# Kernel optimization log

Measured on AMD Instinct MI355X. Metric: run time of the kernel, lower is better.

Reference implementation:

```python
import jax, jax.numpy as jnp
import numpy as np

B, S, E = 2, 2048, 2048
H, D = 16, 128           # n_heads, head_dim (= rope_dim)
BASE = 10000.0


def _rope_tables(seq_len, dim):
    inv_freq = 1.0 / (BASE ** (jnp.arange(0, dim, 2, dtype=jnp.float32) / dim))
    t = jnp.arange(seq_len, dtype=jnp.float32)
    freqs = jnp.outer(t, inv_freq)                 # [S, D/2]
    emb = jnp.concatenate([freqs, freqs], axis=-1)  # [S, D]
    cos = jnp.cos(emb)[None, :, None, :]            # [1, S, 1, D]
    sin = jnp.sin(emb)[None, :, None, :]
    return cos, sin


def _rotate_half(x):
    x1, x2 = x[..., : x.shape[-1] // 2], x[..., x.shape[-1] // 2:]
    return jnp.concatenate([-x2, x1], axis=-1)


def setup_inputs() -> dict:
    key = jax.random.key(0)
    ks = jax.random.split(key, 9)
    s = 1.0 / np.sqrt(E)
    return {
        "x": jax.random.normal(ks[0], (B, S, E), dtype=jnp.float32),
        "Wq": jax.random.uniform(ks[1], (E, E), jnp.float32, -s, s),
        "bq": jax.random.uniform(ks[2], (E,), jnp.float32, -s, s),
        "Wk": jax.random.uniform(ks[3], (E, E), jnp.float32, -s, s),
        "bk": jax.random.uniform(ks[4], (E,), jnp.float32, -s, s),
        "Wv": jax.random.uniform(ks[5], (E, E), jnp.float32, -s, s),
        "bv": jax.random.uniform(ks[6], (E,), jnp.float32, -s, s),
        "Wp": jax.random.uniform(ks[7], (E, E), jnp.float32, -s, s),
        "bp": jax.random.uniform(ks[8], (E,), jnp.float32, -s, s),
    }


def reference(x, Wq, bq, Wk, bk, Wv, bv, Wp, bp):
    b, s, e = x.shape
    # QKV projections (torch Linear: y = x W^T + b)
    q = (jnp.einsum("bse,fe->bsf", x, Wq) + bq).reshape(b, s, H, D)
    k = (jnp.einsum("bse,fe->bsf", x, Wk) + bk).reshape(b, s, H, D)
    v = (jnp.einsum("bse,fe->bsf", x, Wv) + bv).reshape(b, s, H, D)
    # RoPE (rope_dim == head_dim, start_pos = 0)
    cos, sin = _rope_tables(s, D)
    q = q * cos + _rotate_half(q) * sin
    k = k * cos + _rotate_half(k) * sin
    # attention scores [b, m, n, h]
    att = jnp.einsum("bmhd,bnhd->bmnh", q, k)
    causal = jnp.tril(jnp.ones((s, s), dtype=bool))[None, :, :, None]
    att = jnp.where(causal, att, -jnp.inf)
    att = jax.nn.softmax(att / np.sqrt(D), axis=2)
    out = jnp.einsum("bmnh,bnhd->bmhd", att, v).reshape(b, s, e)
    return jnp.einsum("bse,fe->bsf", out, Wp) + bp
```

## Files before the change

kernel.cpp:

```cpp
#include <hip/hip_runtime.h>
#include <hip/hip_bf16.h>
#include <math.h>

#define BB 2
#define SS 2048
#define EE 2048
#define HH 16
#define DD 128
#define MM (BB*SS)

typedef __attribute__((ext_vector_type(8))) short bf16x8;
typedef __attribute__((ext_vector_type(4))) float f32x4;
typedef __attribute__((ext_vector_type(16))) float f32x16;
typedef __attribute__((ext_vector_type(4))) unsigned u32x4;

__device__ inline float bf2f(const __hip_bfloat16 h){ return __bfloat162float(h); }
__device__ inline __hip_bfloat16 f2bf(float f){ return __float2bfloat16(f); }
__device__ inline short f2bs(float f){
  union { __hip_bfloat16 h; short s; } u; u.h = __float2bfloat16(f); return u.s;
}
__device__ inline unsigned pk2(float a, float b){
  union { __hip_bfloat162 h2; unsigned u; } x;
  x.h2 = __float22bfloat162_rn(float2{a,b}); return x.u;
}

__device__ inline void gload16(const void* g, void* l){
  __builtin_amdgcn_global_load_lds((const __attribute__((address_space(1))) void*)g,
      (__attribute__((address_space(3))) void*)l, 16, 0, 0);
}

__global__ void cvt_kernel(const float* __restrict__ in, __hip_bfloat16* __restrict__ out, int n4){
  int i = blockIdx.x*256 + threadIdx.x;
  if (i >= n4) return;
  float4 v = ((const float4*)in)[i];
  union { short4 s4; short s[4]; } u;
  u.s[0] = f2bs(v.x); u.s[1] = f2bs(v.y); u.s[2] = f2bs(v.z); u.s[3] = f2bs(v.w);
  ((short4*)out)[i] = u.s4;
}

struct P4 { const float* s0; const float* s1; const float* s2; const float* s3;
            __hip_bfloat16* d0; __hip_bfloat16* d1; __hip_bfloat16* d2; __hip_bfloat16* d3; };
__global__ void cvt4_kernel(P4 p, int n4){
  int w = blockIdx.y;
  const float* in = w==0 ? p.s0 : w==1 ? p.s1 : w==2 ? p.s2 : p.s3;
  __hip_bfloat16* out = w==0 ? p.d0 : w==1 ? p.d1 : w==2 ? p.d2 : p.d3;
  int i = blockIdx.x*256 + threadIdx.x;
  if (i >= n4) return;
  float4 v = ((const float4*)in)[i];
  union { short4 s4; short s[4]; } u;
  u.s[0] = f2bs(v.x); u.s[1] = f2bs(v.y); u.s[2] = f2bs(v.z); u.s[3] = f2bs(v.w);
  ((short4*)out)[i] = u.s4;
}

__global__ void rope_tables_kernel(float* __restrict__ cost, float* __restrict__ sint){
  int idx = blockIdx.x*256 + threadIdx.x;
  int s = idx >> 6, i = idx & 63;
  double inv = exp(-log(10000.0) * (double)i / 64.0);
  double f = (double)s * inv;
  cost[idx] = (float)cos(f);
  sint[idx] = (float)sin(f);
}

__global__ void rope_kernel(__hip_bfloat16* __restrict__ q, __hip_bfloat16* __restrict__ k,
                            const float* __restrict__ cost, const float* __restrict__ sint){
  int idx = blockIdx.x*256 + threadIdx.x;
  int i = idx & 63;
  int h = (idx >> 6) & (HH-1);
  int bs = idx >> 10;
  int s = bs & (SS-1);
  float c = cost[s*64 + i], sn = sint[s*64 + i];
  size_t base = ((size_t)bs*HH + h)*DD + i;
  float q1 = bf2f(q[base]), q2 = bf2f(q[base+64]);
  q[base]    = f2bf(q1*c - q2*sn);
  q[base+64] = f2bf(q2*c + q1*sn);
  float k1 = bf2f(k[base]), k2 = bf2f(k[base+64]);
  k[base]    = f2bf(k1*c - k2*sn);
  k[base+64] = f2bf(k2*c + k1*sn);
}

template<int MODE>
__global__ __launch_bounds__(512) void gemm256(const __hip_bfloat16* __restrict__ A,
        const __hip_bfloat16* __restrict__ Bw, const float* __restrict__ bias,
        void* __restrict__ Cout){
  __shared__ __align__(1024) char lds[98304];
  const int tid = threadIdx.x, wid = tid>>6, lane = tid&63, g = lane>>4, c16 = lane&15;
  const int wm = wid>>2, wn = wid&3;
  const int orig = blockIdx.x;
  const int wg = (orig & 7)*32 + (orig >> 3);
  const int bm = wg & 31, bn = wg >> 5;
  const int rowA0 = bm*128, rowB0 = bn*256;
  const char* Ab8 = (const char*)A + (size_t)rowA0*4096;
  const char* Bb8 = (const char*)Bw + (size_t)rowB0*4096;

  f32x4 acc[4][4] = {};

  auto stage = [&](int t, int b){
    char* ad = lds + b*49152;
    char* bd = lds + b*49152 + 16384;
    #pragma unroll
    for (int i=0;i<2;i++){
      int off = i*8192 + tid*16;
      int r = off >> 7;
      int cs = (off & 127) ^ ((r&7)<<4);
      gload16(Ab8 + (size_t)r*4096 + t*128 + cs, ad + i*8192 + wid*1024);
    }
    #pragma unroll
    for (int i=0;i<4;i++){
      int off = i*8192 + tid*16;
      int r = off >> 7;
      int cs = (off & 127) ^ ((r&7)<<4);
      gload16(Bb8 + (size_t)r*4096 + t*128 + cs, bd + i*8192 + wid*1024);
    }
  };

  auto compute = [&](int b){
    const char* Abuf = lds + b*49152;
    const char* Bbuf = lds + b*49152 + 16384;
    bf16x8 bfr[4][2];
    #pragma unroll
    for (int ni=0;ni<4;ni++){
      int r = wn*64 + ni*16 + c16;
      int sw = (r&7)<<4;
      #pragma unroll
      for (int kk=0;kk<2;kk++)
        bfr[ni][kk] = *(const bf16x8*)(Bbuf + r*128 + ((kk*64 + g*16) ^ sw));
    }
    #pragma unroll
    for (int mi=0;mi<4;mi++){
      int r = wm*64 + mi*16 + c16;
      int sw = (r&7)<<4;
      bf16x8 af0 = *(const bf16x8*)(Abuf + r*128 + ((g*16) ^ sw));
      bf16x8 af1 = *(const bf16x8*)(Abuf + r*128 + ((64 + g*16) ^ sw));
      __builtin_amdgcn_s_setprio(1);
      #pragma unroll
      for (int ni=0;ni<4;ni++){
        acc[mi][ni] = __builtin_amdgcn_mfma_f32_16x16x32_bf16(af0, bfr[ni][0], acc[mi][ni],0,0,0);
        acc[mi][ni] = __builtin_amdgcn_mfma_f32_16x16x32_bf16(af1, bfr[ni][1], acc[mi][ni],0,0,0);
      }
      __builtin_amdgcn_s_setprio(0);
    }
  };

  stage(0,0);
  stage(1,1);
  asm volatile("s_waitcnt vmcnt(6)" ::: "memory");
  asm volatile("s_barrier" ::: "memory");

  #pragma unroll 1
  for (int tt = 0; tt < 32; tt += 2){
    compute(0);
    asm volatile("s_barrier" ::: "memory");
    if (tt + 2 < 32){ stage(tt+2, 0); asm volatile("s_waitcnt vmcnt(6)" ::: "memory"); }
    else            {                 asm volatile("s_waitcnt vmcnt(0)" ::: "memory"); }
    asm volatile("s_barrier" ::: "memory");
    compute(1);
    if (tt + 2 < 32){
      asm volatile("s_barrier" ::: "memory");
      if (tt + 3 < 32){ stage(tt+3, 1); asm volatile("s_waitcnt vmcnt(6)" ::: "memory"); }
      else            {                 asm volatile("s_waitcnt vmcnt(0)" ::: "memory"); }
      asm volatile("s_barrier" ::: "memory");
    }
  }

  #pragma unroll
  for (int mi=0;mi<4;mi++){
    #pragma unroll
    for (int ni=0;ni<4;ni++){
      int f = rowB0 + wn*64 + ni*16 + c16;
      float bv = bias[f];
      #pragma unroll
      for (int j=0;j<4;j++){
        int m = rowA0 + wm*64 + mi*16 + g*4 + j;
        float v = acc[mi][ni][j] + bv;
        if constexpr (MODE == 0) {
          ((__hip_bfloat16*)Cout)[(size_t)m*EE + f] = f2bf(v);
        } else if constexpr (MODE == 1) {
          int b = m >> 11, s = m & (SS-1);
          ((__hip_bfloat16*)Cout)[((size_t)(b*EE + f))*SS + s] = f2bf(v);
        } else {
          ((float*)Cout)[(size_t)m*EE + f] = v;
        }
      }
    }
  }
}

__global__ __launch_bounds__(256, 2) void attn_kernel(const __hip_bfloat16* __restrict__ qg,
    const __hip_bfloat16* __restrict__ kg, const __hip_bfloat16* __restrict__ vtg,
    __hip_bfloat16* __restrict__ og){
  __shared__ short Ks[2][64*128];
  __shared__ short Vs[2][128*64];
  const int tid=threadIdx.x, wid=tid>>6, lane=tid&63;
  const int c32 = lane & 31, hi = lane >> 5;
  const int id = blockIdx.x;
  const int u = id & 255;
  const int bh = u & 31, pr = u >> 5;
  const int qtile = (id < 256) ? (15 - pr) : pr;
  const int b = bh >> 4, h = bh & 15;
  const int q0 = qtile*128, qw = q0 + wid*32;
  const int qglob = qw + c32;
  const int niter = 2*qtile + 2;

  const char* kb8 = (const char*)(kg + ((size_t)b*SS)*EE + h*DD);
  const char* vb8 = (const char*)(vtg + (size_t)bh*DD*SS);
  const float SCL = 0.08838834764831845f * 1.4426950408889634f;

  const char* qrow = (const char*)(qg + ((size_t)(b*SS + qglob))*EE + h*DD);
  bf16x8 qf[8];
  #pragma unroll
  for (int s=0;s<8;s++) qf[s] = *(const bf16x8*)(qrow + s*32 + hi*16);

  f32x16 pacc[4] = {};
  float mrun = -INFINITY, lrun = 0.f;

  auto stageK = [&](int kv, int buf){
    #pragma unroll
    for (int i=0;i<4;i++){
      int base = i*4096 + wid*1024;
      int lb = base + lane*16;
      int r = lb >> 8, cb = lb & 255;
      gload16(kb8 + (size_t)(kv + r)*4096 + (cb ^ ((r&7)<<4)), (char*)Ks[buf] + base);
    }
  };
  auto stageV = [&](int kv, int buf){
    #pragma unroll
    for (int i=0;i<4;i++){
      int base = i*4096 + wid*1024;
      int lb = base + lane*16;
      int d = lb >> 7, cb = lb & 127;
      gload16(vb8 + (size_t)d*4096 + (size_t)kv*2 + (cb ^ ((d&7)<<4)), (char*)Vs[buf] + base);
    }
  };

  stageK(0,0); stageV(0,0);
  __syncthreads();

  int cur = 0;
  #pragma unroll 1
  for (int it = 0; it < niter; ++it){
    const int kv0 = it*64;
    if (it + 1 < niter){ stageK(kv0+64, cur^1); stageV(kv0+64, cur^1); }

    f32x16 st0 = {}, st1 = {};
    {
      const char* Kb = (const char*)Ks[cur];
      const int sw = (c32 & 7) << 4;
      #pragma unroll
      for (int s=0;s<8;s++){
        bf16x8 kf0 = *(const bf16x8*)(Kb + c32*256        + ((s*32 + hi*16) ^ sw));
        bf16x8 kf1 = *(const bf16x8*)(Kb + (32+c32)*256   + ((s*32 + hi*16) ^ sw));
        st0 = __builtin_amdgcn_mfma_f32_32x32x16_bf16(kf0, qf[s], st0, 0,0,0);
        st1 = __builtin_amdgcn_mfma_f32_32x32x16_bf16(kf1, qf[s], st1, 0,0,0);
      }
    }

    float p[32];
    float vmax = -INFINITY;
    const bool domask = (kv0 + 63 > qw);
    #pragma unroll
    for (int r=0;r<16;r++){
      float v0 = st0[r], v1 = st1[r];
      if (domask){
        int kvo = (r&3) + 8*(r>>2) + 4*hi;
        if (kv0 + kvo > qglob)      v0 = -INFINITY;
        if (kv0 + 32 + kvo > qglob) v1 = -INFINITY;
      }
      p[r] = v0; p[16+r] = v1;
      vmax = fmaxf(vmax, fmaxf(v0, v1));
    }
    vmax = fmaxf(vmax, __shfl_xor(vmax, 32));
    const float mnew = fmaxf(mrun, vmax);
    const float rs = exp2f((mrun - mnew)*SCL);
    mrun = mnew;
    float ps = 0.f;
    #pragma unroll
    for (int i=0;i<32;i++){
      p[i] = exp2f((p[i] - mnew)*SCL);
      ps += p[i];
    }
    ps += __shfl_xor(ps, 32);
    lrun = lrun*rs + ps;

    #pragma unroll
    for (int ds=0; ds<4; ds++)
      #pragma unroll
      for (int r=0;r<16;r++) pacc[ds][r] *= rs;

    unsigned w[2][4][2];
    #pragma unroll
    for (int T=0;T<2;T++)
      #pragma unroll
      for (int m=0;m<4;m++)
        #pragma unroll
        for (int uu=0;uu<2;uu++)
          w[T][m][uu] = pk2(p[T*16 + 4*m + 2*uu], p[T*16 + 4*m + 2*uu + 1]);

    bf16x8 pf[4];
    #pragma unroll
    for (int ks=0; ks<4; ks++){
      int T = ks>>1, lo2 = (ks&1)*2;
      unsigned o0 = hi ? w[T][lo2+1][0] : w[T][lo2+0][0];
      unsigned o1 = hi ? w[T][lo2+1][1] : w[T][lo2+0][1];
      unsigned s0 = hi ? w[T][lo2+0][0] : w[T][lo2+1][0];
      unsigned s1 = hi ? w[T][lo2+0][1] : w[T][lo2+1][1];
      unsigned r0 = (unsigned)__shfl_xor((int)s0, 32);
      unsigned r1 = (unsigned)__shfl_xor((int)s1, 32);
      union { u32x4 u4; bf16x8 h8; } cvt;
      cvt.u4[0] = hi ? r0 : o0;
      cvt.u4[1] = hi ? r1 : o1;
      cvt.u4[2] = hi ? o0 : r0;
      cvt.u4[3] = hi ? o1 : r1;
      pf[ks] = cvt.h8;
    }

    {
      const char* Vb = (const char*)Vs[cur];
      const int vsw = (c32 & 7) << 4;
      #pragma unroll
      for (int ds=0; ds<4; ds++){
        const char* vr = Vb + (ds*32 + c32)*128;
        #pragma unroll
        for (int ks=0; ks<4; ks++){
          bf16x8 vf = *(const bf16x8*)(vr + ((ks*32 + hi*16) ^ vsw));
          pacc[ds] = __builtin_amdgcn_mfma_f32_32x32x16_bf16(vf, pf[ks], pacc[ds], 0,0,0);
        }
      }
    }

    __syncthreads();
    cur ^= 1;
  }

  const float invl = 1.0f / lrun;
  char* orow = (char*)(og + ((size_t)(b*SS + qglob))*EE + h*DD);
  #pragma unroll
  for (int ds=0; ds<4; ds++){
    #pragma unroll
    for (int m=0;m<4;m++){
      int d0 = ds*32 + 8*m + 4*hi;
      short4 s4;
      s4.x = f2bs(pacc[ds][4*m+0]*invl);
      s4.y = f2bs(pacc[ds][4*m+1]*invl);
      s4.z = f2bs(pacc[ds][4*m+2]*invl);
      s4.w = f2bs(pacc[ds][4*m+3]*invl);
      *(short4*)(orow + d0*2) = s4;
    }
  }
}

extern "C" void kernel_launch(void* const* d_in, const int* in_sizes, int n_in,
                              void* d_out, int out_size, void* d_ws, size_t ws_size,
                              hipStream_t stream){
  const float* x  = (const float*)d_in[0];
  const float* Wq = (const float*)d_in[1];
  const float* bq = (const float*)d_in[2];
  const float* Wk = (const float*)d_in[3];
  const float* bk = (const float*)d_in[4];
  const float* Wv = (const float*)d_in[5];
  const float* bv = (const float*)d_in[6];
  const float* Wp = (const float*)d_in[7];
  const float* bp = (const float*)d_in[8];
  float* out = (float*)d_out;

  char* ws = (char*)d_ws;
  size_t off = 0;
  auto alloc = [&](size_t bytes){ void* p = ws + off; off += (bytes + 255) & ~(size_t)255; return p; };
  const size_t nx = (size_t)MM*EE;
  const size_t nw = (size_t)EE*EE;
  __hip_bfloat16* xb  = (__hip_bfloat16*)alloc(nx*2);
  __hip_bfloat16* wqb = (__hip_bfloat16*)alloc(nw*2);
  __hip_bfloat16* wkb = (__hip_bfloat16*)alloc(nw*2);
  __hip_bfloat16* wvb = (__hip_bfloat16*)alloc(nw*2);
  __hip_bfloat16* wpb = (__hip_bfloat16*)alloc(nw*2);
  __hip_bfloat16* qb  = (__hip_bfloat16*)alloc(nx*2);
  __hip_bfloat16* kb  = (__hip_bfloat16*)alloc(nx*2);
  __hip_bfloat16* vtb = (__hip_bfloat16*)alloc(nx*2);
  __hip_bfloat16* ob  = (__hip_bfloat16*)alloc(nx*2);
  float* cost = (float*)alloc((size_t)SS*64*4);
  float* sint = (float*)alloc((size_t)SS*64*4);

  cvt_kernel<<<(int)(nx/4/256), 256, 0, stream>>>(x, xb, (int)(nx/4));
  P4 p4{Wq, Wk, Wv, Wp, wqb, wkb, wvb, wpb};
  cvt4_kernel<<<dim3((int)(nw/4/256), 4), 256, 0, stream>>>(p4, (int)(nw/4));
  rope_tables_kernel<<<SS*64/256, 256, 0, stream>>>(cost, sint);

  gemm256<0><<<256, 512, 0, stream>>>(xb, wqb, bq, qb);
  gemm256<0><<<256, 512, 0, stream>>>(xb, wkb, bk, kb);
  gemm256<1><<<256, 512, 0, stream>>>(xb, wvb, bv, vtb);

  rope_kernel<<<(BB*SS*HH*64)/256, 256, 0, stream>>>(qb, kb, cost, sint);

  attn_kernel<<<dim3(512), 256, 0, stream>>>(qb, kb, vtb, ob);

  gemm256<2><<<256, 512, 0, stream>>>(ob, wpb, bp, out);
}
```

Measured before the change: 284.6 us.

## Widen attention blocks to 256 queries with paired causal tiles per block

The attention kernel now launches 256 blocks of 512 threads (8 waves). Each block covers a 256-row query tile and loops over two tiles (pp and 7-pp) so every block has balanced causal work. This doubles K/V reuse per shared-memory stage and removes the old split into 512 blocks. It also skips the online-softmax rescale when no wave lane sees a new max, and splits the exp-sum into four partial accumulators. The cost is fewer resident blocks per CU and a larger pipeline prologue per tile.

```diff
diff --git a/kernel.cpp b/kernel.cpp
--- a/kernel.cpp
+++ b/kernel.cpp
@@ -185,7 +185,7 @@
   }
 }
 
-__global__ __launch_bounds__(256, 2) void attn_kernel(const __hip_bfloat16* __restrict__ qg,
+__global__ __launch_bounds__(512, 1) void attn_kernel(const __hip_bfloat16* __restrict__ qg,
     const __hip_bfloat16* __restrict__ kg, const __hip_bfloat16* __restrict__ vtg,
     __hip_bfloat16* __restrict__ og){
   __shared__ short Ks[2][64*128];
@@ -193,30 +193,17 @@
   const int tid=threadIdx.x, wid=tid>>6, lane=tid&63;
   const int c32 = lane & 31, hi = lane >> 5;
   const int id = blockIdx.x;
-  const int u = id & 255;
-  const int bh = u & 31, pr = u >> 5;
-  const int qtile = (id < 256) ? (15 - pr) : pr;
+  const int bh = id & 31, pp = id >> 5;
   const int b = bh >> 4, h = bh & 15;
-  const int q0 = qtile*128, qw = q0 + wid*32;
-  const int qglob = qw + c32;
-  const int niter = 2*qtile + 2;
 
   const char* kb8 = (const char*)(kg + ((size_t)b*SS)*EE + h*DD);
   const char* vb8 = (const char*)(vtg + (size_t)bh*DD*SS);
   const float SCL = 0.08838834764831845f * 1.4426950408889634f;
 
-  const char* qrow = (const char*)(qg + ((size_t)(b*SS + qglob))*EE + h*DD);
-  bf16x8 qf[8];
-  #pragma unroll
-  for (int s=0;s<8;s++) qf[s] = *(const bf16x8*)(qrow + s*32 + hi*16);
-
-  f32x16 pacc[4] = {};
-  float mrun = -INFINITY, lrun = 0.f;
-
   auto stageK = [&](int kv, int buf){
     #pragma unroll
-    for (int i=0;i<4;i++){
-      int base = i*4096 + wid*1024;
+    for (int i=0;i<2;i++){
+      int base = i*8192 + wid*1024;
       int lb = base + lane*16;
       int r = lb >> 8, cb = lb & 255;
       gload16(kb8 + (size_t)(kv + r)*4096 + (cb ^ ((r&7)<<4)), (char*)Ks[buf] + base);
@@ -224,127 +211,153 @@
   };
   auto stageV = [&](int kv, int buf){
     #pragma unroll
-    for (int i=0;i<4;i++){
-      int base = i*4096 + wid*1024;
+    for (int i=0;i<2;i++){
+      int base = i*8192 + wid*1024;
       int lb = base + lane*16;
       int d = lb >> 7, cb = lb & 127;
       gload16(vb8 + (size_t)d*4096 + (size_t)kv*2 + (cb ^ ((d&7)<<4)), (char*)Vs[buf] + base);
     }
   };
 
-  stageK(0,0); stageV(0,0);
-  __syncthreads();
-
-  int cur = 0;
   #pragma unroll 1
-  for (int it = 0; it < niter; ++it){
-    const int kv0 = it*64;
-    if (it + 1 < niter){ stageK(kv0+64, cur^1); stageV(kv0+64, cur^1); }
-
-    f32x16 st0 = {}, st1 = {};
-    {
-      const char* Kb = (const char*)Ks[cur];
-      const int sw = (c32 & 7) << 4;
-      #pragma unroll
-      for (int s=0;s<8;s++){
-        bf16x8 kf0 = *(const bf16x8*)(Kb + c32*256        + ((s*32 + hi*16) ^ sw));
-        bf16x8 kf1 = *(const bf16x8*)(Kb + (32+c32)*256   + ((s*32 + hi*16) ^ sw));
-        st0 = __builtin_amdgcn_mfma_f32_32x32x16_bf16(kf0, qf[s], st0, 0,0,0);
-        st1 = __builtin_amdgcn_mfma_f32_32x32x16_bf16(kf1, qf[s], st1, 0,0,0);
-      }
-    }
-
-    float p[32];
-    float vmax = -INFINITY;
-    const bool domask = (kv0 + 63 > qw);
-    #pragma unroll
-    for (int r=0;r<16;r++){
-      float v0 = st0[r], v1 = st1[r];
-      if (domask){
-        int kvo = (r&3) + 8*(r>>2) + 4*hi;
-        if (kv0 + kvo > qglob)      v0 = -INFINITY;
-        if (kv0 + 32 + kvo > qglob) v1 = -INFINITY;
-      }
-      p[r] = v0; p[16+r] = v1;
-      vmax = fmaxf(vmax, fmaxf(v0, v1));
-    }
-    vmax = fmaxf(vmax, __shfl_xor(vmax, 32));
-    const float mnew = fmaxf(mrun, vmax);
-    const float rs = exp2f((mrun - mnew)*SCL);
-    mrun = mnew;
-    float ps = 0.f;
-    #pragma unroll
-    for (int i=0;i<32;i++){
-      p[i] = exp2f((p[i] - mnew)*SCL);
-      ps += p[i];
-    }
-    ps += __shfl_xor(ps, 32);
-    lrun = lrun*rs + ps;
-
-    #pragma unroll
-    for (int ds=0; ds<4; ds++)
-      #pragma unroll
-      for (int r=0;r<16;r++) pacc[ds][r] *= rs;
-
-    unsigned w[2][4][2];
-    #pragma unroll
-    for (int T=0;T<2;T++)
-      #pragma unroll
-      for (int m=0;m<4;m++)
+  for (int tt = 0; tt < 2; ++tt){
+    const int qtile = tt ? (7 - pp) : pp;
+    const int q0 = qtile*256, qw = q0 + wid*32;
+    const int qglob = qw + c32;
+    const int niter = 4*(qtile + 1);
+
+    const char* qrow = (const char*)(qg + ((size_t)(b*SS + qglob))*EE + h*DD);
+    bf16x8 qf[8];
+    #pragma unroll
+    for (int s=0;s<8;s++) qf[s] = *(const bf16x8*)(qrow + s*32 + hi*16);
+
+    f32x16 pacc[4] = {};
+    float mrun = -INFINITY, lrun = 0.f;
+
+    stageK(0,0); stageV(0,0);
+    __syncthreads();
+
+    int cur = 0;
+    #pragma unroll 1
+    for (int it = 0; it < niter; ++it){
+      const int kv0 = it*64;
+      if (it + 1 < niter){ stageK(kv0+64, cur^1); stageV(kv0+64, cur^1); }
+
+      f32x16 st0 = {}, st1 = {};
+      {
+        const char* Kb = (const char*)Ks[cur];
+        const int sw = (c32 & 7) << 4;
         #pragma unroll
-        for (int uu=0;uu<2;uu++)
-          w[T][m][uu] = pk2(p[T*16 + 4*m + 2*uu], p[T*16 + 4*m + 2*uu + 1]);
-
-    bf16x8 pf[4];
-    #pragma unroll
-    for (int ks=0; ks<4; ks++){
-      int T = ks>>1, lo2 = (ks&1)*2;
-      unsigned o0 = hi ? w[T][lo2+1][0] : w[T][lo2+0][0];
-      unsigned o1 = hi ? w[T][lo2+1][1] : w[T][lo2+0][1];
-      unsigned s0 = hi ? w[T][lo2+0][0] : w[T][lo2+1][0];
-      unsigned s1 = hi ? w[T][lo2+0][1] : w[T][lo2+1][1];
-      unsigned r0 = (unsigned)__shfl_xor((int)s0, 32);
-      unsigned r1 = (unsigned)__shfl_xor((int)s1, 32);
-      union { u32x4 u4; bf16x8 h8; } cvt;
-      cvt.u4[0] = hi ? r0 : o0;
-      cvt.u4[1] = hi ? r1 : o1;
-      cvt.u4[2] = hi ? o0 : r0;
-      cvt.u4[3] = hi ? o1 : r1;
-      pf[ks] = cvt.h8;
-    }
-
-    {
-      const char* Vb = (const char*)Vs[cur];
-      const int vsw = (c32 & 7) << 4;
-      #pragma unroll
-      for (int ds=0; ds<4; ds++){
-        const char* vr = Vb + (ds*32 + c32)*128;
+        for (int s=0;s<8;s++){
+          bf16x8 kf0 = *(const bf16x8*)(Kb + c32*256        + ((s*32 + hi*16) ^ sw));
+          bf16x8 kf1 = *(const bf16x8*)(Kb + (32+c32)*256   + ((s*32 + hi*16) ^ sw));
+          st0 = __builtin_amdgcn_mfma_f32_32x32x16_bf16(kf0, qf[s], st0, 0,0,0);
+          st1 = __builtin_amdgcn_mfma_f32_32x32x16_bf16(kf1, qf[s], st1, 0,0,0);
+        }
+      }
+
+      float p[32];
+      float vmax = -INFINITY;
+      const bool domask = (kv0 + 63 > qw);
+      #pragma unroll
+      for (int r=0;r<16;r++){
+        float v0 = st0[r], v1 = st1[r];
+        if (domask){
+          int kvo = (r&3) + 8*(r>>2) + 4*hi;
+          if (kv0 + kvo > qglob)      v0 = -INFINITY;
+          if (kv0 + 32 + kvo > qglob) v1 = -INFINITY;
+        }
+        p[r] = v0; p[16+r] = v1;
+        vmax = fmaxf(vmax, fmaxf(v0, v1));
+      }
+      vmax = fmaxf(vmax, __shfl_xor(vmax, 32));
+
+      const bool anynew = !__all(vmax <= mrun);
+      float mnew = mrun;
+      if (anynew){
+        mnew = fmaxf(mrun, vmax);
+        const float rs = exp2f((mrun - mnew)*SCL);
+        mrun = mnew;
+        lrun *= rs;
         #pragma unroll
-        for (int ks=0; ks<4; ks++){
-          bf16x8 vf = *(const bf16x8*)(vr + ((ks*32 + hi*16) ^ vsw));
-          pacc[ds] = __builtin_amdgcn_mfma_f32_32x32x16_bf16(vf, pf[ks], pacc[ds], 0,0,0);
+        for (int ds=0; ds<4; ds++)
+          #pragma unroll
+          for (int r=0;r<16;r++) pacc[ds][r] *= rs;
+      }
+
+      float s0=0.f, s1=0.f, s2=0.f, s3=0.f;
+      #pragma unroll
+      for (int i=0;i<8;i++){
+        p[i]    = exp2f((p[i]    - mnew)*SCL); s0 += p[i];
+        p[8+i]  = exp2f((p[8+i]  - mnew)*SCL); s1 += p[8+i];
+        p[16+i] = exp2f((p[16+i] - mnew)*SCL); s2 += p[16+i];
+        p[24+i] = exp2f((p[24+i] - mnew)*SCL); s3 += p[24+i];
+      }
+      float ps = (s0 + s1) + (s2 + s3);
+      ps += __shfl_xor(ps, 32);
+      lrun += ps;
+
+      unsigned w[2][4][2];
+      #pragma unroll
+      for (int T=0;T<2;T++)
+        #pragma unroll
+        for (int m=0;m<4;m++)
+          #pragma unroll
+          for (int uu=0;uu<2;uu++)
+            w[T][m][uu] = pk2(p[T*16 + 4*m + 2*uu], p[T*16 + 4*m + 2*uu + 1]);
+
+      bf16x8 pf[4];
+      #pragma unroll
+      for (int ks=0; ks<4; ks++){
+        int T = ks>>1, lo2 = (ks&1)*2;
+        unsigned o0 = hi ? w[T][lo2+1][0] : w[T][lo2+0][0];
+        unsigned o1 = hi ? w[T][lo2+1][1] : w[T][lo2+0][1];
+        unsigned x0 = hi ? w[T][lo2+0][0] : w[T][lo2+1][0];
+        unsigned x1 = hi ? w[T][lo2+0][1] : w[T][lo2+1][1];
+        unsigned r0 = (unsigned)__shfl_xor((int)x0, 32);
+        unsigned r1 = (unsigned)__shfl_xor((int)x1, 32);
+        union { u32x4 u4; bf16x8 h8; } cvt;
+        cvt.u4[0] = hi ? r0 : o0;
+        cvt.u4[1] = hi ? r1 : o1;
+        cvt.u4[2] = hi ? o0 : r0;
+        cvt.u4[3] = hi ? o1 : r1;
+        pf[ks] = cvt.h8;
+      }
+
+      {
+        const char* Vb = (const char*)Vs[cur];
+        const int vsw = (c32 & 7) << 4;
+        #pragma unroll
+        for (int ds=0; ds<4; ds++){
+          const char* vr = Vb + (ds*32 + c32)*128;
+          #pragma unroll
+          for (int ks=0; ks<4; ks++){
+            bf16x8 vf = *(const bf16x8*)(vr + ((ks*32 + hi*16) ^ vsw));
+            pacc[ds] = __builtin_amdgcn_mfma_f32_32x32x16_bf16(vf, pf[ks], pacc[ds], 0,0,0);
+          }
         }
       }
-    }
-
+
+      __syncthreads();
+      cur ^= 1;
+    }
+
+    const float invl = 1.0f / lrun;
+    char* orow = (char*)(og + ((size_t)(b*SS + qglob))*EE + h*DD);
+    #pragma unroll
+    for (int ds=0; ds<4; ds++){
+      #pragma unroll
+      for (int m=0;m<4;m++){
+        int d0 = ds*32 + 8*m + 4*hi;
+        short4 s4;
+        s4.x = f2bs(pacc[ds][4*m+0]*invl);
+        s4.y = f2bs(pacc[ds][4*m+1]*invl);
+        s4.z = f2bs(pacc[ds][4*m+2]*invl);
+        s4.w = f2bs(pacc[ds][4*m+3]*invl);
+        *(short4*)(orow + d0*2) = s4;
+      }
+    }
     __syncthreads();
-    cur ^= 1;
-  }
-
-  const float invl = 1.0f / lrun;
-  char* orow = (char*)(og + ((size_t)(b*SS + qglob))*EE + h*DD);
-  #pragma unroll
-  for (int ds=0; ds<4; ds++){
-    #pragma unroll
-    for (int m=0;m<4;m++){
-      int d0 = ds*32 + 8*m + 4*hi;
-      short4 s4;
-      s4.x = f2bs(pacc[ds][4*m+0]*invl);
-      s4.y = f2bs(pacc[ds][4*m+1]*invl);
-      s4.z = f2bs(pacc[ds][4*m+2]*invl);
-      s4.w = f2bs(pacc[ds][4*m+3]*invl);
-      *(short4*)(orow + d0*2) = s4;
-    }
   }
 }
 
@@ -390,7 +403,7 @@
 
   rope_kernel<<<(BB*SS*HH*64)/256, 256, 0, stream>>>(qb, kb, cost, sint);
 
-  attn_kernel<<<dim3(512), 256, 0, stream>>>(qb, kb, vtb, ob);
+  attn_kernel<<<dim3(256), 512, 0, stream>>>(qb, kb, vtb, ob);
 
   gemm256<2><<<256, 512, 0, stream>>>(ob, wpb, bp, out);
 }
```

New measurement: 333.5 us. 17.2% more time.

## Fuse QKV projections into one GEMM and streamline attention softmax

Applied to the files above, without the earlier changes.

Replaces the three separate Q, K and V projection GEMM launches with one 768-block launch. It relies on the Q, K and V weights and outputs sitting back to back in the workspace, and on a new small kernel that concatenates the three biases. The softmax scale and log2(e) are folded into Q during RoPE, so the attention kernel no longer multiplies scores by a scale. The accumulator rescale is skipped when no lane sees a new maximum, and the exp-sum is split into four independent accumulators. MFMA sections are wrapped in s_setprio to favour matrix work, at the cost of relying on workspace layout and of extra rounding from scaling Q before the bf16 store.

```diff
diff --git a/kernel.cpp b/kernel.cpp
--- a/kernel.cpp
+++ b/kernel.cpp
@@ -28,6 +28,8 @@
   __builtin_amdgcn_global_load_lds((const __attribute__((address_space(1))) void*)g,
       (__attribute__((address_space(3))) void*)l, 16, 0, 0);
 }
+
+#define QSCL 0.12754614533018515f
 
 __global__ void cvt_kernel(const float* __restrict__ in, __hip_bfloat16* __restrict__ out, int n4){
   int i = blockIdx.x*256 + threadIdx.x;
@@ -52,6 +54,13 @@
   ((short4*)out)[i] = u.s4;
 }
 
+__global__ void bcat_kernel(const float* __restrict__ bq, const float* __restrict__ bk,
+                            const float* __restrict__ bv, float* __restrict__ o){
+  int i = blockIdx.x*256 + threadIdx.x;
+  float v = (i < 2048) ? bq[i] : (i < 4096) ? bk[i-2048] : bv[i-4096];
+  o[i] = v;
+}
+
 __global__ void rope_tables_kernel(float* __restrict__ cost, float* __restrict__ sint){
   int idx = blockIdx.x*256 + threadIdx.x;
   int s = idx >> 6, i = idx & 63;
@@ -71,8 +80,8 @@
   float c = cost[s*64 + i], sn = sint[s*64 + i];
   size_t base = ((size_t)bs*HH + h)*DD + i;
   float q1 = bf2f(q[base]), q2 = bf2f(q[base+64]);
-  q[base]    = f2bf(q1*c - q2*sn);
-  q[base+64] = f2bf(q2*c + q1*sn);
+  q[base]    = f2bf((q1*c - q2*sn)*QSCL);
+  q[base+64] = f2bf((q2*c + q1*sn)*QSCL);
   float k1 = bf2f(k[base]), k2 = bf2f(k[base+64]);
   k[base]    = f2bf(k1*c - k2*sn);
   k[base+64] = f2bf(k2*c + k1*sn);
@@ -86,7 +95,8 @@
   const int tid = threadIdx.x, wid = tid>>6, lane = tid&63, g = lane>>4, c16 = lane&15;
   const int wm = wid>>2, wn = wid&3;
   const int orig = blockIdx.x;
-  const int wg = (orig & 7)*32 + (orig >> 3);
+  const int q8 = (int)gridDim.x >> 3;
+  const int wg = (orig & 7)*q8 + (orig >> 3);
   const int bm = wg & 31, bn = wg >> 5;
   const int rowA0 = bm*128, rowB0 = bn*256;
   const char* Ab8 = (const char*)A + (size_t)rowA0*4096;
@@ -177,8 +187,18 @@
         } else if constexpr (MODE == 1) {
           int b = m >> 11, s = m & (SS-1);
           ((__hip_bfloat16*)Cout)[((size_t)(b*EE + f))*SS + s] = f2bf(v);
+        } else if constexpr (MODE == 2) {
+          ((float*)Cout)[(size_t)m*EE + f] = v;
         } else {
-          ((float*)Cout)[(size_t)m*EE + f] = v;
+          __hip_bfloat16* base = (__hip_bfloat16*)Cout;
+          int sec = f >> 11;
+          int fl  = f & 2047;
+          if (sec == 2){
+            int b = m >> 11, s = m & (SS-1);
+            base[(size_t)2*MM*EE + ((size_t)(b*EE + fl))*SS + s] = f2bf(v);
+          } else {
+            base[(size_t)sec*MM*EE + (size_t)m*EE + fl] = f2bf(v);
+          }
         }
       }
     }
@@ -203,7 +223,6 @@
 
   const char* kb8 = (const char*)(kg + ((size_t)b*SS)*EE + h*DD);
   const char* vb8 = (const char*)(vtg + (size_t)bh*DD*SS);
-  const float SCL = 0.08838834764831845f * 1.4426950408889634f;
 
   const char* qrow = (const char*)(qg + ((size_t)(b*SS + qglob))*EE + h*DD);
   bf16x8 qf[8];
@@ -245,6 +264,7 @@
     {
       const char* Kb = (const char*)Ks[cur];
       const int sw = (c32 & 7) << 4;
+      __builtin_amdgcn_s_setprio(1);
       #pragma unroll
       for (int s=0;s<8;s++){
         bf16x8 kf0 = *(const bf16x8*)(Kb + c32*256        + ((s*32 + hi*16) ^ sw));
@@ -252,6 +272,7 @@
         st0 = __builtin_amdgcn_mfma_f32_32x32x16_bf16(kf0, qf[s], st0, 0,0,0);
         st1 = __builtin_amdgcn_mfma_f32_32x32x16_bf16(kf1, qf[s], st1, 0,0,0);
       }
+      __builtin_amdgcn_s_setprio(0);
     }
 
     float p[32];
@@ -269,22 +290,31 @@
       vmax = fmaxf(vmax, fmaxf(v0, v1));
     }
     vmax = fmaxf(vmax, __shfl_xor(vmax, 32));
-    const float mnew = fmaxf(mrun, vmax);
-    const float rs = exp2f((mrun - mnew)*SCL);
-    mrun = mnew;
-    float ps = 0.f;
-    #pragma unroll
-    for (int i=0;i<32;i++){
-      p[i] = exp2f((p[i] - mnew)*SCL);
-      ps += p[i];
-    }
+
+    const bool anynew = !__all(vmax <= mrun);
+    float mnew = mrun;
+    if (anynew){
+      mnew = fmaxf(mrun, vmax);
+      const float rs = exp2f(mrun - mnew);
+      mrun = mnew;
+      lrun *= rs;
+      #pragma unroll
+      for (int ds=0; ds<4; ds++)
+        #pragma unroll
+        for (int r=0;r<16;r++) pacc[ds][r] *= rs;
+    }
+
+    float s0=0.f, s1=0.f, s2=0.f, s3=0.f;
+    #pragma unroll
+    for (int i=0;i<8;i++){
+      p[i]    = exp2f(p[i]    - mnew); s0 += p[i];
+      p[8+i]  = exp2f(p[8+i]  - mnew); s1 += p[8+i];
+      p[16+i] = exp2f(p[16+i] - mnew); s2 += p[16+i];
+      p[24+i] = exp2f(p[24+i] - mnew); s3 += p[24+i];
+    }
+    float ps = (s0 + s1) + (s2 + s3);
     ps += __shfl_xor(ps, 32);
-    lrun = lrun*rs + ps;
-
-    #pragma unroll
-    for (int ds=0; ds<4; ds++)
-      #pragma unroll
-      for (int r=0;r<16;r++) pacc[ds][r] *= rs;
+    lrun += ps;
 
     unsigned w[2][4][2];
     #pragma unroll
@@ -301,10 +331,10 @@
       int T = ks>>1, lo2 = (ks&1)*2;
       unsigned o0 = hi ? w[T][lo2+1][0] : w[T][lo2+0][0];
       unsigned o1 = hi ? w[T][lo2+1][1] : w[T][lo2+0][1];
-      unsigned s0 = hi ? w[T][lo2+0][0] : w[T][lo2+1][0];
-      unsigned s1 = hi ? w[T][lo2+0][1] : w[T][lo2+1][1];
-      unsigned r0 = (unsigned)__shfl_xor((int)s0, 32);
-      unsigned r1 = (unsigned)__shfl_xor((int)s1, 32);
+      unsigned x0 = hi ? w[T][lo2+0][0] : w[T][lo2+1][0];
+      unsigned x1 = hi ? w[T][lo2+0][1] : w[T][lo2+1][1];
+      unsigned r0 = (unsigned)__shfl_xor((int)x0, 32);
+      unsigned r1 = (unsigned)__shfl_xor((int)x1, 32);
       union { u32x4 u4; bf16x8 h8; } cvt;
       cvt.u4[0] = hi ? r0 : o0;
       cvt.u4[1] = hi ? r1 : o1;
@@ -316,6 +346,7 @@
     {
       const char* Vb = (const char*)Vs[cur];
       const int vsw = (c32 & 7) << 4;
+      __builtin_amdgcn_s_setprio(1);
       #pragma unroll
       for (int ds=0; ds<4; ds++){
         const char* vr = Vb + (ds*32 + c32)*128;
@@ -325,6 +356,7 @@
           pacc[ds] = __builtin_amdgcn_mfma_f32_32x32x16_bf16(vf, pf[ks], pacc[ds], 0,0,0);
         }
       }
+      __builtin_amdgcn_s_setprio(0);
     }
 
     __syncthreads();
@@ -378,15 +410,15 @@
   __hip_bfloat16* ob  = (__hip_bfloat16*)alloc(nx*2);
   float* cost = (float*)alloc((size_t)SS*64*4);
   float* sint = (float*)alloc((size_t)SS*64*4);
+  float* bqkv = (float*)alloc((size_t)3*EE*4);
 
   cvt_kernel<<<(int)(nx/4/256), 256, 0, stream>>>(x, xb, (int)(nx/4));
   P4 p4{Wq, Wk, Wv, Wp, wqb, wkb, wvb, wpb};
   cvt4_kernel<<<dim3((int)(nw/4/256), 4), 256, 0, stream>>>(p4, (int)(nw/4));
+  bcat_kernel<<<24, 256, 0, stream>>>(bq, bk, bv, bqkv);
   rope_tables_kernel<<<SS*64/256, 256, 0, stream>>>(cost, sint);
 
-  gemm256<0><<<256, 512, 0, stream>>>(xb, wqb, bq, qb);
-  gemm256<0><<<256, 512, 0, stream>>>(xb, wkb, bk, kb);
-  gemm256<1><<<256, 512, 0, stream>>>(xb, wvb, bv, vtb);
+  gemm256<3><<<768, 512, 0, stream>>>(xb, wqb, bqkv, qb);
 
   rope_kernel<<<(BB*SS*HH*64)/256, 256, 0, stream>>>(qb, kb, cost, sint);
 
```

Measured after the change: 315.1 us. 10.7% more time.
